# Kernel optimization log

Hardware: AMD Instinct MI355X
Metric: run time of the kernel (lower is better)

Reference implementation:

```python
import jax, jax.numpy as jnp
import numpy as np

# Model config (matches init_kwargs)
B, I, H, C = 2048, 1024, 2048, 1000   # batch, input_dim, hidden_dim, num_classes
S = 8                                  # num_wavefunctions
TOPK = 256
PARTIAL_NORM = 1.0
SM_STEPS = 2                           # self_modulation_steps
EPS = 1e-8


def setup_inputs() -> dict:
    key = jax.random.key(0)
    ks = jax.random.split(key, 9)
    x      = jax.random.normal(ks[0], (B, I), jnp.float32)
    # stacked per-wavefunction Linear(input_dim, 2*hidden_dim)
    W      = jax.random.normal(ks[1], (S, 2 * H, I), jnp.float32) * (1.0 / np.sqrt(I))
    b      = jax.random.normal(ks[2], (S, 2 * H), jnp.float32) * 0.01
    phases = jax.random.normal(ks[3], (S, H), jnp.float32) * 0.1   # phase_per_dim=True
    gate_W = jax.random.normal(ks[4], (H, H), jnp.float32) * (1.0 / np.sqrt(H))
    gate_b = jax.random.normal(ks[5], (H,), jnp.float32) * 0.01
    clf_W  = jax.random.normal(ks[6], (C, H), jnp.float32) * (1.0 / np.sqrt(H))
    clf_b  = jax.random.normal(ks[7], (C,), jnp.float32) * 0.01
    return {"x": x, "W": W, "b": b, "phases": phases,
            "gate_W": gate_W, "gate_b": gate_b, "clf_W": clf_W, "clf_b": clf_b}


def reference(x, W, b, phases, gate_W, gate_b, clf_W, clf_b):
    # All wavefunction branches batched into one GEMM: [B,S,2H]
    out = jnp.einsum('bi,shi->bsh', x, W) + b[None]
    out = jnp.exp(-(out * out))                      # ArcBell activation
    alpha, beta = out[..., :H], out[..., H:]         # [B,S,H] each
    norm_sq = jnp.sum(alpha * alpha + beta * beta, axis=-1, keepdims=True) + EPS
    factor = jnp.sqrt((PARTIAL_NORM * PARTIAL_NORM) / norm_sq)  # [B,S,1]
    alpha = alpha * factor
    beta = beta * factor
    cphi = jnp.cos(phases)[None]                     # [1,S,H]
    sphi = jnp.sin(phases)[None]
    # phase rotation + complex accumulate over wavefunctions
    sup_real = jnp.sum(alpha * cphi - beta * sphi, axis=1)   # [B,H]
    sup_imag = jnp.sum(alpha * sphi + beta * cphi, axis=1)
    # self-modulation (fixed small step count -> Python loop is fine)
    for _ in range(SM_STEPS):
        mag = jnp.sqrt(sup_real * sup_real + sup_imag * sup_imag)
        gate = jax.nn.sigmoid(mag @ gate_W.T + gate_b)
        sup_real = sup_real * gate
        sup_imag = sup_imag * gate
    mag_sq = sup_real * sup_real + sup_imag * sup_imag       # [B,H]
    # top-k masked probability aggregation
    _, idx = jax.lax.top_k(mag_sq, TOPK)                     # idx: [B,TOPK]
    mask = jnp.zeros_like(mag_sq).at[jnp.arange(B)[:, None], idx].set(1.0)
    masked = mag_sq * mask
    probs = masked / (jnp.sum(masked, axis=-1, keepdims=True) + EPS)
    logits = probs @ clf_W.T + clf_b                         # [B,C]
    return logits
```

## Files before the change

kernel.cpp:

```cpp
#include <hip/hip_runtime.h>

typedef _Float16 f16;
typedef _Float16 f16x8 __attribute__((ext_vector_type(8)));
typedef _Float16 f16x4 __attribute__((ext_vector_type(4)));
typedef float f32x4 __attribute__((ext_vector_type(4)));

#define B_    2048
#define I_    1024
#define H_    2048
#define C_    1000
#define S_    8
#define N1    32768
#define TOPK_ 256

__device__ __forceinline__ void gload16(const void* g, void* l) {
  __builtin_amdgcn_global_load_lds((const __attribute__((address_space(1))) void*)g,
                                   (__attribute__((address_space(3))) void*)l,
                                   16, 0, 0);
}

__global__ void cvt8_kernel(const float* __restrict__ src, f16* __restrict__ dst, int n8) {
  int i = blockIdx.x * blockDim.x + threadIdx.x;
  if (i >= n8) return;
  const float4 a = reinterpret_cast<const float4*>(src)[2 * i];
  const float4 b = reinterpret_cast<const float4*>(src)[2 * i + 1];
  f16x8 o = { (f16)a.x, (f16)a.y, (f16)a.z, (f16)a.w,
              (f16)b.x, (f16)b.y, (f16)b.z, (f16)b.w };
  reinterpret_cast<f16x8*>(dst)[i] = o;
}

__global__ void cvt_clf_kernel(const float* __restrict__ src, f16* __restrict__ dst) {
  int i = blockIdx.x * blockDim.x + threadIdx.x;
  if (i >= (1024 * H_ / 8)) return;
  f16x8 o;
  if (i < (C_ * H_ / 8)) {
    const float4 a = reinterpret_cast<const float4*>(src)[2 * i];
    const float4 b = reinterpret_cast<const float4*>(src)[2 * i + 1];
    o = (f16x8){ (f16)a.x, (f16)a.y, (f16)a.z, (f16)a.w,
                 (f16)b.x, (f16)b.y, (f16)b.z, (f16)b.w };
  } else {
    o = (f16x8){ (f16)0.f, (f16)0.f, (f16)0.f, (f16)0.f,
                 (f16)0.f, (f16)0.f, (f16)0.f, (f16)0.f };
  }
  reinterpret_cast<f16x8*>(dst)[i] = o;
}

__global__ void phase_kernel(const float* __restrict__ ph, float* __restrict__ c,
                             float* __restrict__ s) {
  int i = blockIdx.x * blockDim.x + threadIdx.x;
  if (i >= S_ * H_) return;
  float p = ph[i];
  c[i] = cosf(p);
  s[i] = sinf(p);
}

__global__ __launch_bounds__(512, 1)
void gemm1_8p(const f16* __restrict__ A, const f16* __restrict__ Bm,
              const float* __restrict__ bias, f16* __restrict__ act)
{
  __shared__ char SL[131072];
  const int tid = threadIdx.x, lane = tid & 63, wid = tid >> 6;
  const int wr = wid >> 2, wc = wid & 3;
  const int fr = lane & 15, fq = lane >> 4;
  const int bid = blockIdx.x;
  const int swz = (bid & 7) * 128 + (bid >> 3);
  const int mt = swz & 7, nt = swz >> 3;
  const long brow = (long)mt * 256, bcol = (long)nt * 256;

  const int schunk = ((tid & 3) ^ ((tid >> 3) & 3)) * 8;
  const f16* sA = A  + (brow + (tid >> 2)) * (long)I_ + schunk;
  const f16* sB = Bm + (bcol + (tid >> 2)) * (long)I_ + schunk;

  const int co = (fq ^ ((fr >> 1) & 3)) * 16;
  const int rdA0 = (wr * 128 + fr) * 64 + co;
  const int rdB0 = 32768 + (wc * 64 + fr) * 64 + co;

  f32x4 acc[8][4] = {};

#define STG(mat, kh, c, tp, buf)                                                \
  gload16(((mat) ? sB : sA) + (size_t)(c) * 128 * I_ + (size_t)(tp) * 64 + (kh) * 32, \
          SL + (buf) * 65536 + (mat) * 32768 + (kh) * 16384 + (c) * 8192 + tid * 16)

  STG(0,0,0,0,0); STG(0,0,1,0,0); STG(1,0,0,0,0); STG(1,0,1,0,0);
  STG(0,1,0,0,0); STG(0,1,1,0,0); STG(1,1,0,0,0); STG(1,1,1,0,0);
  asm volatile("s_waitcnt vmcnt(4)" ::: "memory");
  __builtin_amdgcn_s_barrier();

#pragma unroll 1
  for (int t = 0; t < 16; ++t) {
    const int buf = t & 1, nbuf = buf ^ 1;
    const char* rb = SL + buf * 65536;
    const bool pre = (t < 15);
    f16x8 af[4], bf[4];

    if (pre) { STG(0,0,0,t+1,nbuf); STG(0,0,1,t+1,nbuf); }
#pragma unroll
    for (int n = 0; n < 4; ++n) bf[n] = *(const f16x8*)(rb + rdB0 + n * 1024);
#pragma unroll
    for (int i = 0; i < 4; ++i) af[i] = *(const f16x8*)(rb + rdA0 + i * 1024);
    asm volatile("" ::: "memory");
    __builtin_amdgcn_s_barrier();
    asm volatile("s_waitcnt lgkmcnt(0)" ::: "memory");
    __builtin_amdgcn_s_setprio(1);
#pragma unroll
    for (int i = 0; i < 4; ++i)
#pragma unroll
      for (int n = 0; n < 4; ++n)
        acc[i][n] = __builtin_amdgcn_mfma_f32_16x16x32_f16(af[i], bf[n], acc[i][n], 0, 0, 0);
    __builtin_amdgcn_s_setprio(0);
    asm volatile("" ::: "memory");
    __builtin_amdgcn_s_barrier();

    if (pre) { STG(1,0,0,t+1,nbuf); STG(1,0,1,t+1,nbuf); }
#pragma unroll
    for (int i = 0; i < 4; ++i) af[i] = *(const f16x8*)(rb + rdA0 + (4 + i) * 1024);
    asm volatile("" ::: "memory");
    __builtin_amdgcn_s_barrier();
    asm volatile("s_waitcnt lgkmcnt(0)" ::: "memory");
    __builtin_amdgcn_s_setprio(1);
#pragma unroll
    for (int i = 0; i < 4; ++i)
#pragma unroll
      for (int n = 0; n < 4; ++n)
        acc[4 + i][n] = __builtin_amdgcn_mfma_f32_16x16x32_f16(af[i], bf[n], acc[4 + i][n], 0, 0, 0);
    __builtin_amdgcn_s_setprio(0);
    if (pre) asm volatile("s_waitcnt vmcnt(4)" ::: "memory");
    else     asm volatile("s_waitcnt vmcnt(0)" ::: "memory");
    asm volatile("" ::: "memory");
    __builtin_amdgcn_s_barrier();

    if (pre) { STG(0,1,0,t+1,nbuf); STG(0,1,1,t+1,nbuf); }
#pragma unroll
    for (int n = 0; n < 4; ++n) bf[n] = *(const f16x8*)(rb + 16384 + rdB0 + n * 1024);
#pragma unroll
    for (int i = 0; i < 4; ++i) af[i] = *(const f16x8*)(rb + 16384 + rdA0 + i * 1024);
    asm volatile("" ::: "memory");
    __builtin_amdgcn_s_barrier();
    asm volatile("s_waitcnt lgkmcnt(0)" ::: "memory");
    __builtin_amdgcn_s_setprio(1);
#pragma unroll
    for (int i = 0; i < 4; ++i)
#pragma unroll
      for (int n = 0; n < 4; ++n)
        acc[i][n] = __builtin_amdgcn_mfma_f32_16x16x32_f16(af[i], bf[n], acc[i][n], 0, 0, 0);
    __builtin_amdgcn_s_setprio(0);
    asm volatile("" ::: "memory");
    __builtin_amdgcn_s_barrier();

    if (pre) { STG(1,1,0,t+1,nbuf); STG(1,1,1,t+1,nbuf); }
#pragma unroll
    for (int i = 0; i < 4; ++i) af[i] = *(const f16x8*)(rb + 16384 + rdA0 + (4 + i) * 1024);
    asm volatile("" ::: "memory");
    __builtin_amdgcn_s_barrier();
    asm volatile("s_waitcnt lgkmcnt(0)" ::: "memory");
    __builtin_amdgcn_s_setprio(1);
#pragma unroll
    for (int i = 0; i < 4; ++i)
#pragma unroll
      for (int n = 0; n < 4; ++n)
        acc[4 + i][n] = __builtin_amdgcn_mfma_f32_16x16x32_f16(af[i], bf[n], acc[4 + i][n], 0, 0, 0);
    __builtin_amdgcn_s_setprio(0);
    if (pre) asm volatile("s_waitcnt vmcnt(4)" ::: "memory");
    else     asm volatile("s_waitcnt vmcnt(0)" ::: "memory");
    asm volatile("" ::: "memory");
    __builtin_amdgcn_s_barrier();
  }
#undef STG

  float bv[4];
#pragma unroll
  for (int n = 0; n < 4; ++n) bv[n] = bias[bcol + wc * 64 + n * 16 + fr];
#pragma unroll
  for (int m = 0; m < 8; ++m) {
    const long r0 = brow + wr * 128 + m * 16 + fq * 4;
#pragma unroll
    for (int n = 0; n < 4; ++n) {
      const long c = bcol + wc * 64 + n * 16 + fr;
#pragma unroll
      for (int j = 0; j < 4; ++j) {
        const float tt = acc[m][n][j] + bv[n];
        act[(r0 + j) * (long)N1 + c] = (f16)__expf(-tt * tt);
      }
    }
  }
}

template<int BM, int BN, int WM, int WN, int THREADS, int EPI>
__global__ __launch_bounds__(THREADS, 3)
void gemm_ring(const f16* __restrict__ A, const f16* __restrict__ Bmat,
               const int K, const int MT, const int ldc, const int nreal,
               const float* __restrict__ bias,
               const float* __restrict__ magin,
               float* __restrict__ mago32, f16* __restrict__ mago16,
               float* __restrict__ msqout, float* __restrict__ logits)
{
  constexpr int MREP  = BM / (WM * 16);
  constexpr int NREP  = BN / (WN * 16);
  constexpr int CA    = (BM * 64) / (THREADS * 16);
  constexpr int CB    = (BN * 64) / (THREADS * 16);
  constexpr int CALLS = CA + CB;
  constexpr int SLOT  = (BM + BN) * 32;
  __shared__ f16 SL[4 * SLOT];

  const int tid  = threadIdx.x;
  const int lane = tid & 63, wid = tid >> 6;
  const int wr = wid / WN, wc = wid % WN;
  const int fr = lane & 15, fq = lane >> 4;

  const int nwg = gridDim.x;
  const int chunk = nwg >> 3;
  const int swz = (blockIdx.x & 7) * chunk + (blockIdx.x >> 3);
  const int mt = swz % MT, nt = swz / MT;
  const long brow = (long)mt * BM, bcol = (long)nt * BN;

  const f16* srcA[CA];
  const f16* srcB[CB];
#pragma unroll
  for (int a = 0; a < CA; ++a) {
    const int r = (a * THREADS + tid) >> 2;
    const int cs = (tid & 3) ^ ((r ^ (r >> 2)) & 3);
    srcA[a] = A + (size_t)(brow + r) * K + cs * 8;
  }
#pragma unroll
  for (int a = 0; a < CB; ++a) {
    const int r = (a * THREADS + tid) >> 2;
    const int cs = (tid & 3) ^ ((r ^ (r >> 2)) & 3);
    srcB[a] = Bmat + (size_t)(bcol + r) * K + cs * 8;
  }

  int ard[MREP], brd[NREP];
#pragma unroll
  for (int m = 0; m < MREP; ++m) {
    const int r = wr * MREP * 16 + m * 16 + fr;
    ard[m] = r * 32 + ((fq ^ ((r ^ (r >> 2)) & 3)) * 8);
  }
#pragma unroll
  for (int n = 0; n < NREP; ++n) {
    const int r = wc * NREP * 16 + n * 16 + fr;
    brd[n] = r * 32 + ((fq ^ ((r ^ (r >> 2)) & 3)) * 8);
  }

  f32x4 acc[MREP][NREP] = {};
  const int ntile = K >> 5;

#define STAGE_TILE(tt)                                                         \
  do {                                                                         \
    f16* D = &SL[((tt) & 3) * SLOT];                                           \
    const long kt = (long)(tt) * 32;                                           \
    _Pragma("unroll")                                                          \
    for (int a = 0; a < CA; ++a)                                               \
      gload16(srcA[a] + kt, D + a * THREADS * 8 + wid * 512);                  \
    _Pragma("unroll")                                                          \
    for (int a = 0; a < CB; ++a)                                               \
      gload16(srcB[a] + kt, D + BM * 32 + a * THREADS * 8 + wid * 512);        \
  } while (0)

  STAGE_TILE(0); STAGE_TILE(1); STAGE_TILE(2);

  for (int t = 0; t < ntile; ++t) {
    if (t + 3 < ntile) STAGE_TILE(t + 3);
    if (t < ntile - 3)       asm volatile("s_waitcnt vmcnt(%0)" :: "i"(3 * CALLS) : "memory");
    else if (t == ntile - 3) asm volatile("s_waitcnt vmcnt(%0)" :: "i"(2 * CALLS) : "memory");
    else if (t == ntile - 2) asm volatile("s_waitcnt vmcnt(%0)" :: "i"(1 * CALLS) : "memory");
    else                     asm volatile("s_waitcnt vmcnt(0)" ::: "memory");
    __builtin_amdgcn_s_barrier();
    asm volatile("" ::: "memory");

    const f16* SA = &SL[(t & 3) * SLOT];
    const f16* SB = SA + BM * 32;
    f16x8 af[MREP], bf[NREP];
#pragma unroll
    for (int m = 0; m < MREP; ++m) af[m] = *(const f16x8*)(SA + ard[m]);
#pragma unroll
    for (int n = 0; n < NREP; ++n) bf[n] = *(const f16x8*)(SB + brd[n]);

    __builtin_amdgcn_s_setprio(1);
#pragma unroll
    for (int m = 0; m < MREP; ++m)
#pragma unroll
      for (int n = 0; n < NREP; ++n)
        acc[m][n] = __builtin_amdgcn_mfma_f32_16x16x32_f16(af[m], bf[n], acc[m][n], 0, 0, 0);
    __builtin_amdgcn_s_setprio(0);
    asm volatile("" ::: "memory");
    __builtin_amdgcn_s_barrier();
  }
#undef STAGE_TILE

#pragma unroll
  for (int m = 0; m < MREP; ++m) {
    const long r0 = brow + wr * MREP * 16 + m * 16 + fq * 4;
#pragma unroll
    for (int n = 0; n < NREP; ++n) {
      const long c = bcol + wc * NREP * 16 + n * 16 + fr;
      float bv;
      if (EPI == 2) bv = (c < nreal) ? bias[c] : 0.f;
      else          bv = bias[c];
#pragma unroll
      for (int j = 0; j < 4; ++j) {
        const long r = r0 + j;
        const float t = acc[m][n][j] + bv;
        if (EPI == 1) {
          const float g = 1.f / (1.f + __expf(-t));
          const long idx = r * (long)ldc + c;
          const float v = magin[idx] * g;
          if (msqout) msqout[idx] = v * v;
          else { mago32[idx] = v; mago16[idx] = (f16)v; }
        } else {
          if (c < nreal) logits[r * (long)nreal + c] = t;
        }
      }
    }
  }
}

__global__ __launch_bounds__(512)
void normsup_kernel(const f16* __restrict__ act,
                    const float* __restrict__ cphi, const float* __restrict__ sphi,
                    float* __restrict__ mag32, f16* __restrict__ mag16)
{
  __shared__ float buf[4096];
  __shared__ float red[8];
  const int b = blockIdx.x, tid = threadIdx.x;
  const int lane = tid & 63, wv = tid >> 6;
  float sr[4] = {0, 0, 0, 0}, si[4] = {0, 0, 0, 0};
  const f16* base = act + (size_t)b * N1;

  for (int s = 0; s < S_; ++s) {
    f16x8 v = *(const f16x8*)(base + s * 4096 + tid * 8);
    float ls = 0.f;
#pragma unroll
    for (int e = 0; e < 8; ++e) {
      float f = (float)v[e];
      buf[tid * 8 + e] = f;
      ls += f * f;
    }
#pragma unroll
    for (int o = 32; o > 0; o >>= 1) ls += __shfl_down(ls, o);
    if (lane == 0) red[wv] = ls;
    __syncthreads();
    const float tot = red[0] + red[1] + red[2] + red[3] + red[4] + red[5] + red[6] + red[7];
    const float factor = 1.f / sqrtf(tot + 1e-8f);

    const float4 c4 = *(const float4*)(cphi + s * H_ + tid * 4);
    const float4 s4 = *(const float4*)(sphi + s * H_ + tid * 4);
    const float4 a4 = *(const float4*)(&buf[tid * 4]);
    const float4 b4 = *(const float4*)(&buf[2048 + tid * 4]);
    sr[0] += factor * (a4.x * c4.x - b4.x * s4.x); si[0] += factor * (a4.x * s4.x + b4.x * c4.x);
    sr[1] += factor * (a4.y * c4.y - b4.y * s4.y); si[1] += factor * (a4.y * s4.y + b4.y * c4.y);
    sr[2] += factor * (a4.z * c4.z - b4.z * s4.z); si[2] += factor * (a4.z * s4.z + b4.z * c4.z);
    sr[3] += factor * (a4.w * c4.w - b4.w * s4.w); si[3] += factor * (a4.w * s4.w + b4.w * c4.w);
    __syncthreads();
  }

  const size_t o = (size_t)b * H_ + tid * 4;
  const float m0 = sqrtf(sr[0] * sr[0] + si[0] * si[0]);
  const float m1 = sqrtf(sr[1] * sr[1] + si[1] * si[1]);
  const float m2 = sqrtf(sr[2] * sr[2] + si[2] * si[2]);
  const float m3 = sqrtf(sr[3] * sr[3] + si[3] * si[3]);
  *(float4*)(mag32 + o) = make_float4(m0, m1, m2, m3);
  f16x4 mh = { (f16)m0, (f16)m1, (f16)m2, (f16)m3 };
  *(f16x4*)(mag16 + o) = mh;
}

__global__ __launch_bounds__(256)
void topk_kernel(const float* __restrict__ msq, f16* __restrict__ probs)
{
  __shared__ unsigned vals[2048];
  __shared__ int hist[256];
  __shared__ int scn[256];
  __shared__ int sdig, sknew;
  __shared__ float wsum[4];
  const int b = blockIdx.x, tid = threadIdx.x;
  const unsigned* row = (const unsigned*)(msq + (size_t)b * H_);

  uint4 v0 = *(const uint4*)(row + tid * 8);
  uint4 v1 = *(const uint4*)(row + tid * 8 + 4);
  vals[tid * 8 + 0] = v0.x; vals[tid * 8 + 1] = v0.y;
  vals[tid * 8 + 2] = v0.z; vals[tid * 8 + 3] = v0.w;
  vals[tid * 8 + 4] = v1.x; vals[tid * 8 + 5] = v1.y;
  vals[tid * 8 + 6] = v1.z; vals[tid * 8 + 7] = v1.w;
  __syncthreads();

  int k = TOPK_;
  unsigned prefix = 0, pmask = 0;
  for (int pass = 0; pass < 4; ++pass) {
    const int sh = 24 - pass * 8;
    hist[tid] = 0;
    __syncthreads();
#pragma unroll
    for (int e = 0; e < 8; ++e) {
      unsigned v = vals[tid * 8 + e];
      if ((v & pmask) == prefix) atomicAdd(&hist[(v >> sh) & 255u], 1);
    }
    __syncthreads();
    const int own = hist[tid];
    int sc = own;
    scn[tid] = sc;
    __syncthreads();
    for (int o2 = 1; o2 < 256; o2 <<= 1) {
      int add = (tid + o2 < 256) ? scn[tid + o2] : 0;
      __syncthreads();
      sc += add; scn[tid] = sc;
      __syncthreads();
    }
    if (sc >= k && (sc - own) < k) { sdig = tid; sknew = k - (sc - own); }
    __syncthreads();
    prefix |= ((unsigned)sdig) << sh;
    pmask  |= 0xFFu << sh;
    k = sknew;
    __syncthreads();
  }

  const unsigned T = prefix;
  const int krem = k;
  unsigned vl[8];
  int eqc = 0;
#pragma unroll
  for (int e = 0; e < 8; ++e) { vl[e] = vals[tid * 8 + e]; if (vl[e] == T) eqc++; }
  int sc2 = eqc;
  scn[tid] = sc2;
  __syncthreads();
  for (int o2 = 1; o2 < 256; o2 <<= 1) {
    int add = (tid >= o2) ? scn[tid - o2] : 0;
    __syncthreads();
    sc2 += add; scn[tid] = sc2;
    __syncthreads();
  }
  int rank = sc2 - eqc;
  float ls = 0.f;
  bool sel[8];
#pragma unroll
  for (int e = 0; e < 8; ++e) {
    const unsigned v = vl[e];
    bool s_ = false;
    if (v > T) s_ = true;
    else if (v == T) { s_ = (rank < krem); ++rank; }
    sel[e] = s_;
    if (s_) ls += __uint_as_float(v);
  }
#pragma unroll
  for (int o2 = 32; o2 > 0; o2 >>= 1) ls += __shfl_down(ls, o2);
  if ((tid & 63) == 0) wsum[tid >> 6] = ls;
  __syncthreads();
  const float tot = wsum[0] + wsum[1] + wsum[2] + wsum[3];
  const float inv = 1.f / (tot + 1e-8f);
  f16x8 ov;
#pragma unroll
  for (int e = 0; e < 8; ++e)
    ov[e] = sel[e] ? (f16)(__uint_as_float(vl[e]) * inv) : (f16)0.f;
  *(f16x8*)(probs + (size_t)b * H_ + tid * 8) = ov;
}

extern "C" void kernel_launch(void* const* d_in, const int* in_sizes, int n_in,
                              void* d_out, int out_size, void* d_ws, size_t ws_size,
                              hipStream_t stream)
{
  const float* x  = (const float*)d_in[0];
  const float* W  = (const float*)d_in[1];
  const float* bb = (const float*)d_in[2];
  const float* ph = (const float*)d_in[3];
  const float* gW = (const float*)d_in[4];
  const float* gb = (const float*)d_in[5];
  const float* cW = (const float*)d_in[6];
  const float* cb = (const float*)d_in[7];
  float* out = (float*)d_out;

  char* base = (char*)d_ws;
  size_t off = 0;
  auto take = [&](size_t bytes) -> char* {
    char* r = base + off;
    off += (bytes + 255) & ~(size_t)255;
    return r;
  };
  f16*   Wf    = (f16*)  take((size_t)S_ * 2 * H_ * I_ * 2);
  f16*   xf    = (f16*)  take((size_t)B_ * I_ * 2);
  f16*   gWf   = (f16*)  take((size_t)H_ * H_ * 2);
  f16*   cWf   = (f16*)  take((size_t)1024 * H_ * 2);
  float* cphi  = (float*)take((size_t)S_ * H_ * 4);
  float* sphi  = (float*)take((size_t)S_ * H_ * 4);
  f16*   act   = (f16*)  take((size_t)B_ * N1 * 2);
  float* mag0f = (float*)take((size_t)B_ * H_ * 4);
  f16*   mag0h = (f16*)  take((size_t)B_ * H_ * 2);
  float* mag1f = (float*)take((size_t)B_ * H_ * 4);
  f16*   mag1h = (f16*)  take((size_t)B_ * H_ * 2);
  float* msq   = (float*)take((size_t)B_ * H_ * 4);
  f16*   probs = (f16*)  take((size_t)B_ * H_ * 2);
  (void)ws_size; (void)in_sizes; (void)n_in; (void)out_size;

  cvt8_kernel<<<(S_ * 2 * H_ * I_ / 8 + 255) / 256, 256, 0, stream>>>(W, Wf, S_ * 2 * H_ * I_ / 8);
  cvt8_kernel<<<(B_ * I_ / 8 + 255) / 256, 256, 0, stream>>>(x, xf, B_ * I_ / 8);
  cvt8_kernel<<<(H_ * H_ / 8 + 255) / 256, 256, 0, stream>>>(gW, gWf, H_ * H_ / 8);
  cvt_clf_kernel<<<(1024 * H_ / 8 + 255) / 256, 256, 0, stream>>>(cW, cWf);
  phase_kernel<<<(S_ * H_ + 255) / 256, 256, 0, stream>>>(ph, cphi, sphi);

  gemm1_8p<<<(B_ / 256) * (N1 / 256), 512, 0, stream>>>(xf, Wf, bb, act);

  normsup_kernel<<<B_, 512, 0, stream>>>(act, cphi, sphi, mag0f, mag0h);

  gemm_ring<128, 64, 2, 2, 256, 1><<<(B_ / 128) * (H_ / 64), 256, 0, stream>>>(
      mag0h, gWf, H_, B_ / 128, H_, H_, gb,
      mag0f, mag1f, mag1h, nullptr, nullptr);

  gemm_ring<128, 64, 2, 2, 256, 1><<<(B_ / 128) * (H_ / 64), 256, 0, stream>>>(
      mag1h, gWf, H_, B_ / 128, H_, H_, gb,
      mag1f, nullptr, nullptr, msq, nullptr);

  topk_kernel<<<B_, 256, 0, stream>>>(msq, probs);

  gemm_ring<128, 64, 2, 2, 256, 2><<<(B_ / 128) * (1024 / 64), 256, 0, stream>>>(
      probs, cWf, H_, B_ / 128, 0, C_, cb,
      nullptr, nullptr, nullptr, nullptr, out);
}
```

Measured before the change: 374.9 us.

## Convert main GEMM to a four-slot ring buffer with prefetch depth three

The large first GEMM moves from a double buffer holding 64-wide K tiles to a four-slot ring of 32-wide K tiles, with loads issued three tiles ahead. Each iteration now has half as many barriers, and more loads stay in flight to hide global-memory latency. The smaller ring GEMMs also switch to a simpler XOR swizzle for LDS bank mapping, and their waves-per-EU bound becomes a template parameter. The deeper ring still uses the full 128 KB of LDS, and the vmcnt bookkeeping is more fragile.

```diff
diff --git a/kernel.cpp b/kernel.cpp
--- a/kernel.cpp
+++ b/kernel.cpp
@@ -55,7 +55,7 @@
 }
 
 __global__ __launch_bounds__(512, 1)
-void gemm1_8p(const f16* __restrict__ A, const f16* __restrict__ Bm,
+void gemm1_r4(const f16* __restrict__ A, const f16* __restrict__ Bm,
               const float* __restrict__ bias, f16* __restrict__ act)
 {
   __shared__ char SL[131072];
@@ -68,32 +68,35 @@
   const long brow = (long)mt * 256, bcol = (long)nt * 256;
 
   const int schunk = ((tid & 3) ^ ((tid >> 3) & 3)) * 8;
-  const f16* sA = A  + (brow + (tid >> 2)) * (long)I_ + schunk;
-  const f16* sB = Bm + (bcol + (tid >> 2)) * (long)I_ + schunk;
+  const f16* srcP[4];
+  srcP[0] = A  + (brow + (tid >> 2)) * (long)I_ + schunk;
+  srcP[1] = A  + (brow + 128 + (tid >> 2)) * (long)I_ + schunk;
+  srcP[2] = Bm + (bcol + (tid >> 2)) * (long)I_ + schunk;
+  srcP[3] = Bm + (bcol + 128 + (tid >> 2)) * (long)I_ + schunk;
 
   const int co = (fq ^ ((fr >> 1) & 3)) * 16;
   const int rdA0 = (wr * 128 + fr) * 64 + co;
-  const int rdB0 = 32768 + (wc * 64 + fr) * 64 + co;
+  const int rdB0 = 16384 + (wc * 64 + fr) * 64 + co;
 
   f32x4 acc[8][4] = {};
 
-#define STG(mat, kh, c, tp, buf)                                                \
-  gload16(((mat) ? sB : sA) + (size_t)(c) * 128 * I_ + (size_t)(tp) * 64 + (kh) * 32, \
-          SL + (buf) * 65536 + (mat) * 32768 + (kh) * 16384 + (c) * 8192 + tid * 16)
-
-  STG(0,0,0,0,0); STG(0,0,1,0,0); STG(1,0,0,0,0); STG(1,0,1,0,0);
-  STG(0,1,0,0,0); STG(0,1,1,0,0); STG(1,1,0,0,0); STG(1,1,1,0,0);
-  asm volatile("s_waitcnt vmcnt(4)" ::: "memory");
+#define STG1(a, tt)                                                    \
+  gload16(srcP[a] + (size_t)(tt) * 32,                                 \
+          SL + ((tt) & 3) * 32768 + ((a) * 512 + tid) * 16)
+
+  STG1(0,0); STG1(1,0); STG1(2,0); STG1(3,0);
+  STG1(0,1); STG1(1,1); STG1(2,1); STG1(3,1);
+  STG1(0,2); STG1(1,2); STG1(2,2); STG1(3,2);
+  asm volatile("s_waitcnt vmcnt(8)" ::: "memory");
   __builtin_amdgcn_s_barrier();
 
 #pragma unroll 1
-  for (int t = 0; t < 16; ++t) {
-    const int buf = t & 1, nbuf = buf ^ 1;
-    const char* rb = SL + buf * 65536;
-    const bool pre = (t < 15);
+  for (int t = 0; t < 32; ++t) {
+    const char* rb = SL + (t & 3) * 32768;
+    const bool pre = (t < 29);
     f16x8 af[4], bf[4];
 
-    if (pre) { STG(0,0,0,t+1,nbuf); STG(0,0,1,t+1,nbuf); }
+    if (pre) { STG1(0, t + 3); STG1(1, t + 3); }
 #pragma unroll
     for (int n = 0; n < 4; ++n) bf[n] = *(const f16x8*)(rb + rdB0 + n * 1024);
 #pragma unroll
@@ -111,7 +114,7 @@
     asm volatile("" ::: "memory");
     __builtin_amdgcn_s_barrier();
 
-    if (pre) { STG(1,0,0,t+1,nbuf); STG(1,0,1,t+1,nbuf); }
+    if (pre) { STG1(2, t + 3); STG1(3, t + 3); }
 #pragma unroll
     for (int i = 0; i < 4; ++i) af[i] = *(const f16x8*)(rb + rdA0 + (4 + i) * 1024);
     asm volatile("" ::: "memory");
@@ -124,48 +127,13 @@
       for (int n = 0; n < 4; ++n)
         acc[4 + i][n] = __builtin_amdgcn_mfma_f32_16x16x32_f16(af[i], bf[n], acc[4 + i][n], 0, 0, 0);
     __builtin_amdgcn_s_setprio(0);
-    if (pre) asm volatile("s_waitcnt vmcnt(4)" ::: "memory");
-    else     asm volatile("s_waitcnt vmcnt(0)" ::: "memory");
-    asm volatile("" ::: "memory");
-    __builtin_amdgcn_s_barrier();
-
-    if (pre) { STG(0,1,0,t+1,nbuf); STG(0,1,1,t+1,nbuf); }
-#pragma unroll
-    for (int n = 0; n < 4; ++n) bf[n] = *(const f16x8*)(rb + 16384 + rdB0 + n * 1024);
-#pragma unroll
-    for (int i = 0; i < 4; ++i) af[i] = *(const f16x8*)(rb + 16384 + rdA0 + i * 1024);
-    asm volatile("" ::: "memory");
-    __builtin_amdgcn_s_barrier();
-    asm volatile("s_waitcnt lgkmcnt(0)" ::: "memory");
-    __builtin_amdgcn_s_setprio(1);
-#pragma unroll
-    for (int i = 0; i < 4; ++i)
-#pragma unroll
-      for (int n = 0; n < 4; ++n)
-        acc[i][n] = __builtin_amdgcn_mfma_f32_16x16x32_f16(af[i], bf[n], acc[i][n], 0, 0, 0);
-    __builtin_amdgcn_s_setprio(0);
-    asm volatile("" ::: "memory");
-    __builtin_amdgcn_s_barrier();
-
-    if (pre) { STG(1,1,0,t+1,nbuf); STG(1,1,1,t+1,nbuf); }
-#pragma unroll
-    for (int i = 0; i < 4; ++i) af[i] = *(const f16x8*)(rb + 16384 + rdA0 + (4 + i) * 1024);
-    asm volatile("" ::: "memory");
-    __builtin_amdgcn_s_barrier();
-    asm volatile("s_waitcnt lgkmcnt(0)" ::: "memory");
-    __builtin_amdgcn_s_setprio(1);
-#pragma unroll
-    for (int i = 0; i < 4; ++i)
-#pragma unroll
-      for (int n = 0; n < 4; ++n)
-        acc[4 + i][n] = __builtin_amdgcn_mfma_f32_16x16x32_f16(af[i], bf[n], acc[4 + i][n], 0, 0, 0);
-    __builtin_amdgcn_s_setprio(0);
-    if (pre) asm volatile("s_waitcnt vmcnt(4)" ::: "memory");
-    else     asm volatile("s_waitcnt vmcnt(0)" ::: "memory");
-    asm volatile("" ::: "memory");
-    __builtin_amdgcn_s_barrier();
-  }
-#undef STG
+    if (t < 29)       asm volatile("s_waitcnt vmcnt(8)" ::: "memory");
+    else if (t == 29) asm volatile("s_waitcnt vmcnt(4)" ::: "memory");
+    else              asm volatile("s_waitcnt vmcnt(0)" ::: "memory");
+    asm volatile("" ::: "memory");
+    __builtin_amdgcn_s_barrier();
+  }
+#undef STG1
 
   float bv[4];
 #pragma unroll
@@ -185,8 +153,8 @@
   }
 }
 
-template<int BM, int BN, int WM, int WN, int THREADS, int EPI>
-__global__ __launch_bounds__(THREADS, 3)
+template<int BM, int BN, int WM, int WN, int THREADS, int MINW, int EPI>
+__global__ __launch_bounds__(THREADS, MINW)
 void gemm_ring(const f16* __restrict__ A, const f16* __restrict__ Bmat,
                const int K, const int MT, const int ldc, const int nreal,
                const float* __restrict__ bias,
@@ -218,13 +186,13 @@
 #pragma unroll
   for (int a = 0; a < CA; ++a) {
     const int r = (a * THREADS + tid) >> 2;
-    const int cs = (tid & 3) ^ ((r ^ (r >> 2)) & 3);
+    const int cs = (tid & 3) ^ ((r >> 1) & 3);
     srcA[a] = A + (size_t)(brow + r) * K + cs * 8;
   }
 #pragma unroll
   for (int a = 0; a < CB; ++a) {
     const int r = (a * THREADS + tid) >> 2;
-    const int cs = (tid & 3) ^ ((r ^ (r >> 2)) & 3);
+    const int cs = (tid & 3) ^ ((r >> 1) & 3);
     srcB[a] = Bmat + (size_t)(bcol + r) * K + cs * 8;
   }
 
@@ -232,12 +200,12 @@
 #pragma unroll
   for (int m = 0; m < MREP; ++m) {
     const int r = wr * MREP * 16 + m * 16 + fr;
-    ard[m] = r * 32 + ((fq ^ ((r ^ (r >> 2)) & 3)) * 8);
+    ard[m] = r * 32 + ((fq ^ ((r >> 1) & 3)) * 8);
   }
 #pragma unroll
   for (int n = 0; n < NREP; ++n) {
     const int r = wc * NREP * 16 + n * 16 + fr;
-    brd[n] = r * 32 + ((fq ^ ((r ^ (r >> 2)) & 3)) * 8);
+    brd[n] = r * 32 + ((fq ^ ((r >> 1) & 3)) * 8);
   }
 
   f32x4 acc[MREP][NREP] = {};
@@ -493,21 +461,21 @@
   cvt_clf_kernel<<<(1024 * H_ / 8 + 255) / 256, 256, 0, stream>>>(cW, cWf);
   phase_kernel<<<(S_ * H_ + 255) / 256, 256, 0, stream>>>(ph, cphi, sphi);
 
-  gemm1_8p<<<(B_ / 256) * (N1 / 256), 512, 0, stream>>>(xf, Wf, bb, act);
+  gemm1_r4<<<(B_ / 256) * (N1 / 256), 512, 0, stream>>>(xf, Wf, bb, act);
 
   normsup_kernel<<<B_, 512, 0, stream>>>(act, cphi, sphi, mag0f, mag0h);
 
-  gemm_ring<128, 64, 2, 2, 256, 1><<<(B_ / 128) * (H_ / 64), 256, 0, stream>>>(
+  gemm_ring<128, 64, 2, 2, 256, 3, 1><<<(B_ / 128) * (H_ / 64), 256, 0, stream>>>(
       mag0h, gWf, H_, B_ / 128, H_, H_, gb,
       mag0f, mag1f, mag1h, nullptr, nullptr);
 
-  gemm_ring<128, 64, 2, 2, 256, 1><<<(B_ / 128) * (H_ / 64), 256, 0, stream>>>(
+  gemm_ring<128, 64, 2, 2, 256, 3, 1><<<(B_ / 128) * (H_ / 64), 256, 0, stream>>>(
       mag1h, gWf, H_, B_ / 128, H_, H_, gb,
       mag1f, nullptr, nullptr, msq, nullptr);
 
   topk_kernel<<<B_, 256, 0, stream>>>(msq, probs);
 
-  gemm_ring<128, 64, 2, 2, 256, 2><<<(B_ / 128) * (1024 / 64), 256, 0, stream>>>(
+  gemm_ring<128, 64, 2, 2, 256, 3, 2><<<(B_ / 128) * (1024 / 64), 256, 0, stream>>>(
       probs, cWf, H_, B_ / 128, 0, C_, cb,
       nullptr, nullptr, nullptr, nullptr, out);
 }
```

Result: no change. 374.0 us (-0.2%).
